# Kernel tuning notes

Hardware: AMD Instinct MI355X
Metric: run time of the kernel (lower is better)

The kernel has to match this reference:

```python
import jax, jax.numpy as jnp
import numpy as np

B, IN, OUT, M = 4096, 512, 512, 16


def setup_inputs() -> dict:
    key = jax.random.key(0)
    k1, k2, k3 = jax.random.split(key, 3)
    # inputs kept strictly positive and inside the physical range [0, 60]
    x = jax.random.uniform(k1, (B, IN), jnp.float32, 0.1, 10.0)
    # photonic basis coefficients: positive, with small polynomial terms
    b_coef = jax.random.uniform(k2, (M, 8), jnp.float32, 0.1, 0.9)
    b_coef = b_coef.at[:, 4:].multiply(0.01)
    coeffs = 0.01 * jax.random.normal(k3, (OUT, IN, M), jnp.float32)
    return {"x": x, "coeffs": coeffs, "b_coef": b_coef}


def _photonic_basis(x, b):
    # x: (B, IN) -> broadcast against M basis functions -> (B, IN, M)
    xe = x[:, :, None]                                   # (B, IN, 1)
    b1, b2, b3, b4, b5, b6, b7, b8 = [b[:, i][None, None, :] for i in range(8)]
    inner = jnp.expm1(b3 * xe)
    powered = jnp.power(inner, b4)
    y = (b1 * jnp.log(1.0 + b2 * jnp.log1p(powered))
         + b5 * xe + b6 * xe**2 + b7 * xe**3 + b8 * xe**4)
    return y


def reference(x, coeffs, b_coef):
    # basis: (B, IN, M); double reduce over (IN, M) == GEMM of size B x (IN*M) x OUT
    basis = _photonic_basis(x, b_coef)
    y = jnp.einsum('bim,oim->bo', basis, coeffs)         # (B, OUT)
    return y
```

## Files before the change

kernel.cpp:

```cpp
#include <hip/hip_runtime.h>
#include <hip/hip_bf16.h>
#include <stdint.h>

#define B_DIM   4096
#define IN_DIM  512
#define OUT_DIM 512
#define M_DIM   16
#define K_DIM   (IN_DIM * M_DIM)
#define MN      (B_DIM * OUT_DIM)

typedef unsigned short ushort_t;
typedef __attribute__((ext_vector_type(8))) __bf16 bf16x8;
typedef __attribute__((ext_vector_type(4))) float  f32x4;

__device__ __forceinline__ ushort_t f2bf(float f) {
  union { float f; uint32_t u; } v; v.f = f;
  uint32_t u = v.u + 0x7fffu + ((v.u >> 16) & 1u);
  return (ushort_t)(u >> 16);
}

__global__ __launch_bounds__(256) void convert_coeffs_kernel(
    const float* __restrict__ src, ushort_t* __restrict__ dst, int n4) {
  int i = blockIdx.x * 256 + threadIdx.x;
  if (i >= n4) return;
  float4 v = ((const float4*)src)[i];
  ushort4 o;
  o.x = f2bf(v.x); o.y = f2bf(v.y); o.z = f2bf(v.z); o.w = f2bf(v.w);
  ((ushort4*)dst)[i] = o;
}

__global__ __launch_bounds__(256) void basis_kernel(
    const float* __restrict__ x, const float* __restrict__ bc,
    ushort_t* __restrict__ basis) {
  int idx = blockIdx.x * 256 + threadIdx.x;
  float xv = x[idx];
  float x2 = xv * xv, x3 = x2 * xv, x4 = x2 * x2;
  const float LOG2E = 1.44269504088896340736f;
  const float LN2   = 0.69314718055994530942f;
  uint32_t w[8];
  #pragma unroll
  for (int m = 0; m < 16; ++m) {
    float b1 = bc[m*8+0], b2 = bc[m*8+1], b3 = bc[m*8+2], b4 = bc[m*8+3];
    float b5 = bc[m*8+4], b6 = bc[m*8+5], b7 = bc[m*8+6], b8 = bc[m*8+7];
    float e     = __builtin_amdgcn_exp2f(b3 * xv * LOG2E);
    float inner = e - 1.0f;
    float p     = __builtin_amdgcn_exp2f(b4 * __builtin_amdgcn_logf(inner));
    float u     = LN2 * __builtin_amdgcn_logf(1.0f + p);
    float vv    = LN2 * __builtin_amdgcn_logf(1.0f + b2 * u);
    float y = b1 * vv + b5 * xv + b6 * x2 + b7 * x3 + b8 * x4;
    uint32_t h = (uint32_t)f2bf(y);
    if (m & 1) w[m >> 1] |= (h << 16); else w[m >> 1] = h;
  }
  uint4* dst = (uint4*)(basis + (size_t)idx * 16);
  dst[0] = make_uint4(w[0], w[1], w[2], w[3]);
  dst[1] = make_uint4(w[4], w[5], w[6], w[7]);
}

#define BM 128
#define BN 128
#define BK 32
#define SPLITK 4
#define KC (K_DIM / SPLITK)

#define GLD16(g, l) \
  __builtin_amdgcn_global_load_lds((const __attribute__((address_space(1))) void*)(g), \
                                   (__attribute__((address_space(3))) void*)(l), 16, 0, 0)

template <int ATOMIC>
__global__ __launch_bounds__(256, 2) void gemm_kernel(
    const ushort_t* __restrict__ A,
    const ushort_t* __restrict__ Bt,
    float* __restrict__ P) {
  __shared__ __align__(16) ushort_t As[BM * BK];
  __shared__ __align__(16) ushort_t Bs[BN * BK];
  const int tid  = threadIdx.x;
  const int wave = tid >> 6;
  const int lane = tid & 63;
  const int bm = blockIdx.x, bn = blockIdx.y, ks = blockIdx.z;

  const int srow = wave * 16 + (lane >> 2);
  const int scol = (lane & 3) * 8;
  const ushort_t* Ag  = A  + (size_t)(bm * BM + srow) * K_DIM + (size_t)ks * KC + scol;
  const ushort_t* Bg  = Bt + (size_t)(bn * BN + srow) * K_DIM + (size_t)ks * KC + scol;
  const ushort_t* Ag2 = Ag + (size_t)64 * K_DIM;
  const ushort_t* Bg2 = Bg + (size_t)64 * K_DIM;
  ushort_t* AsW  = As + wave * 16 * BK;
  ushort_t* AsW2 = AsW + 64 * BK;
  ushort_t* BsW  = Bs + wave * 16 * BK;
  ushort_t* BsW2 = BsW + 64 * BK;

  const int wr = wave >> 1, wc = wave & 1;
  const int fm = lane & 15;
  const int fk = (lane >> 4) * 8;

  f32x4 acc[4][4] = {};

  for (int kt = 0; kt < KC; kt += BK) {
    GLD16(Ag, AsW); GLD16(Ag2, AsW2);
    GLD16(Bg, BsW); GLD16(Bg2, BsW2);
    Ag += BK; Ag2 += BK; Bg += BK; Bg2 += BK;
    __syncthreads();
    bf16x8 af[4], bfv[4];
    #pragma unroll
    for (int t = 0; t < 4; ++t) {
      af[t]  = *(const bf16x8*)(As + (wr * 64 + t * 16 + fm) * BK + fk);
      bfv[t] = *(const bf16x8*)(Bs + (wc * 64 + t * 16 + fm) * BK + fk);
    }
    #pragma unroll
    for (int mt = 0; mt < 4; ++mt)
      #pragma unroll
      for (int nt = 0; nt < 4; ++nt)
        acc[mt][nt] = __builtin_amdgcn_mfma_f32_16x16x32_bf16(af[mt], bfv[nt], acc[mt][nt], 0, 0, 0);
    __syncthreads();
  }

  const int colb = bn * BN + wc * 64 + fm;
  const int rowb = bm * BM + wr * 64 + (lane >> 4) * 4;
  float* out = P + (ATOMIC ? (size_t)0 : (size_t)ks * MN);
  #pragma unroll
  for (int mt = 0; mt < 4; ++mt) {
    #pragma unroll
    for (int nt = 0; nt < 4; ++nt) {
      #pragma unroll
      for (int j = 0; j < 4; ++j) {
        int row = rowb + mt * 16 + j;
        int col = colb + nt * 16;
        float vv = acc[mt][nt][j];
        if (ATOMIC) atomicAdd(out + (size_t)row * OUT_DIM + col, vv);
        else        out[(size_t)row * OUT_DIM + col] = vv;
      }
    }
  }
}

__global__ __launch_bounds__(256) void reduce_kernel(
    const float* __restrict__ P, float* __restrict__ out) {
  int i = blockIdx.x * 256 + threadIdx.x;
  const float4* p = (const float4*)P;
  float4 a = p[i], b = p[i + MN/4], c = p[i + 2*(MN/4)], d = p[i + 3*(MN/4)];
  float4 r = make_float4(a.x + b.x + c.x + d.x, a.y + b.y + c.y + d.y,
                         a.z + b.z + c.z + d.z, a.w + b.w + c.w + d.w);
  ((float4*)out)[i] = r;
}

extern "C" void kernel_launch(void* const* d_in, const int* in_sizes, int n_in,
                              void* d_out, int out_size, void* d_ws, size_t ws_size,
                              hipStream_t stream) {
  const float* x      = (const float*)d_in[0];
  const float* coeffs = (const float*)d_in[1];
  const float* b_coef = (const float*)d_in[2];
  float* out = (float*)d_out;
  char*  ws  = (char*)d_ws;

  const size_t BASIS_BYTES = (size_t)B_DIM * K_DIM * 2;
  const size_t COEF_BYTES  = (size_t)OUT_DIM * K_DIM * 2;
  ushort_t* basis = (ushort_t*)ws;
  ushort_t* coefb = (ushort_t*)(ws + BASIS_BYTES);
  float* partials = (float*)(ws + BASIS_BYTES + COEF_BYTES);
  const size_t FULL = BASIS_BYTES + COEF_BYTES + (size_t)SPLITK * MN * 4;
  const bool use_atomic = (ws_size < FULL);

  convert_coeffs_kernel<<<(OUT_DIM * K_DIM / 4 + 255) / 256, 256, 0, stream>>>(
      coeffs, coefb, OUT_DIM * K_DIM / 4);
  basis_kernel<<<(B_DIM * IN_DIM) / 256, 256, 0, stream>>>(x, b_coef, basis);

  dim3 grid(B_DIM / BM, OUT_DIM / BN, SPLITK);
  if (use_atomic) {
    hipMemsetAsync(d_out, 0, (size_t)MN * 4, stream);
    gemm_kernel<1><<<grid, 256, 0, stream>>>(basis, coefb, out);
  } else {
    gemm_kernel<0><<<grid, 256, 0, stream>>>(basis, coefb, partials);
    reduce_kernel<<<MN / 4 / 256, 256, 0, stream>>>(partials, out);
  }
}
```

Before: 148.3 us.

## Process two inputs per basis thread, raise split-K, remap LDS tile layout

The basis kernel now computes two x values per thread, interleaving their transcendental chains to expose more instruction-level parallelism, and uses half as many threads. The GEMM's LDS layout changes so each wave loads contiguous 16-row by 32-k groups that map directly onto MFMA fragment reads (lane*8), aiming to reduce LDS bank conflicts. Split-K doubles from 4 to 8 to give the GEMM more blocks, and the reduce kernel is generalized to loop over SPLITK. The higher split-K doubles partial-sum traffic and reduce work, or doubles atomic contention on the fallback path.

```diff
diff --git a/kernel.cpp b/kernel.cpp
--- a/kernel.cpp
+++ b/kernel.cpp
@@ -29,37 +29,49 @@
   ((ushort4*)dst)[i] = o;
 }
 
-__global__ __launch_bounds__(256) void basis_kernel(
+__global__ __launch_bounds__(256, 1) void basis_kernel(
     const float* __restrict__ x, const float* __restrict__ bc,
     ushort_t* __restrict__ basis) {
-  int idx = blockIdx.x * 256 + threadIdx.x;
-  float xv = x[idx];
-  float x2 = xv * xv, x3 = x2 * xv, x4 = x2 * x2;
+  int idx2 = blockIdx.x * 256 + threadIdx.x;
+  float2 xp = ((const float2*)x)[idx2];
+  float x0 = xp.x, x1 = xp.y;
+  float p0_2 = x0 * x0, p0_3 = p0_2 * x0, p0_4 = p0_2 * p0_2;
+  float p1_2 = x1 * x1, p1_3 = p1_2 * x1, p1_4 = p1_2 * p1_2;
   const float LOG2E = 1.44269504088896340736f;
   const float LN2   = 0.69314718055994530942f;
-  uint32_t w[8];
+  uint32_t w0[8], w1[8];
   #pragma unroll
   for (int m = 0; m < 16; ++m) {
     float b1 = bc[m*8+0], b2 = bc[m*8+1], b3 = bc[m*8+2], b4 = bc[m*8+3];
     float b5 = bc[m*8+4], b6 = bc[m*8+5], b7 = bc[m*8+6], b8 = bc[m*8+7];
-    float e     = __builtin_amdgcn_exp2f(b3 * xv * LOG2E);
-    float inner = e - 1.0f;
-    float p     = __builtin_amdgcn_exp2f(b4 * __builtin_amdgcn_logf(inner));
-    float u     = LN2 * __builtin_amdgcn_logf(1.0f + p);
-    float vv    = LN2 * __builtin_amdgcn_logf(1.0f + b2 * u);
-    float y = b1 * vv + b5 * xv + b6 * x2 + b7 * x3 + b8 * x4;
-    uint32_t h = (uint32_t)f2bf(y);
-    if (m & 1) w[m >> 1] |= (h << 16); else w[m >> 1] = h;
+    float e0 = __builtin_amdgcn_exp2f(b3 * x0 * LOG2E);
+    float e1 = __builtin_amdgcn_exp2f(b3 * x1 * LOG2E);
+    float l0 = __builtin_amdgcn_logf(e0 - 1.0f);
+    float l1 = __builtin_amdgcn_logf(e1 - 1.0f);
+    float q0 = __builtin_amdgcn_exp2f(b4 * l0);
+    float q1 = __builtin_amdgcn_exp2f(b4 * l1);
+    float u0 = LN2 * __builtin_amdgcn_logf(1.0f + q0);
+    float u1 = LN2 * __builtin_amdgcn_logf(1.0f + q1);
+    float v0 = LN2 * __builtin_amdgcn_logf(1.0f + b2 * u0);
+    float v1 = LN2 * __builtin_amdgcn_logf(1.0f + b2 * u1);
+    float y0 = b1 * v0 + b5 * x0 + b6 * p0_2 + b7 * p0_3 + b8 * p0_4;
+    float y1 = b1 * v1 + b5 * x1 + b6 * p1_2 + b7 * p1_3 + b8 * p1_4;
+    uint32_t h0 = (uint32_t)f2bf(y0);
+    uint32_t h1 = (uint32_t)f2bf(y1);
+    if (m & 1) { w0[m >> 1] |= (h0 << 16); w1[m >> 1] |= (h1 << 16); }
+    else       { w0[m >> 1] = h0;          w1[m >> 1] = h1; }
   }
-  uint4* dst = (uint4*)(basis + (size_t)idx * 16);
-  dst[0] = make_uint4(w[0], w[1], w[2], w[3]);
-  dst[1] = make_uint4(w[4], w[5], w[6], w[7]);
+  uint4* dst = (uint4*)(basis + (size_t)idx2 * 32);
+  dst[0] = make_uint4(w0[0], w0[1], w0[2], w0[3]);
+  dst[1] = make_uint4(w0[4], w0[5], w0[6], w0[7]);
+  dst[2] = make_uint4(w1[0], w1[1], w1[2], w1[3]);
+  dst[3] = make_uint4(w1[4], w1[5], w1[6], w1[7]);
 }
 
 #define BM 128
 #define BN 128
 #define BK 32
-#define SPLITK 4
+#define SPLITK 8
 #define KC (K_DIM / SPLITK)
 
 #define GLD16(g, l) \
@@ -78,33 +90,33 @@
   const int lane = tid & 63;
   const int bm = blockIdx.x, bn = blockIdx.y, ks = blockIdx.z;
 
-  const int srow = wave * 16 + (lane >> 2);
-  const int scol = (lane & 3) * 8;
-  const ushort_t* Ag  = A  + (size_t)(bm * BM + srow) * K_DIM + (size_t)ks * KC + scol;
-  const ushort_t* Bg  = Bt + (size_t)(bn * BN + srow) * K_DIM + (size_t)ks * KC + scol;
-  const ushort_t* Ag2 = Ag + (size_t)64 * K_DIM;
-  const ushort_t* Bg2 = Bg + (size_t)64 * K_DIM;
-  ushort_t* AsW  = As + wave * 16 * BK;
-  ushort_t* AsW2 = AsW + 64 * BK;
-  ushort_t* BsW  = Bs + wave * 16 * BK;
-  ushort_t* BsW2 = BsW + 64 * BK;
+  const int grow = lane & 15;
+  const int koct = lane >> 4;
+  const int g0 = 2 * wave, g1 = 2 * wave + 1;
+  const ushort_t* Ag0 = A  + (size_t)(bm * BM + g0 * 16 + grow) * K_DIM + (size_t)ks * KC + koct * 8;
+  const ushort_t* Ag1 = A  + (size_t)(bm * BM + g1 * 16 + grow) * K_DIM + (size_t)ks * KC + koct * 8;
+  const ushort_t* Bg0 = Bt + (size_t)(bn * BN + g0 * 16 + grow) * K_DIM + (size_t)ks * KC + koct * 8;
+  const ushort_t* Bg1 = Bt + (size_t)(bn * BN + g1 * 16 + grow) * K_DIM + (size_t)ks * KC + koct * 8;
+  ushort_t* AsW0 = As + g0 * 512;
+  ushort_t* AsW1 = As + g1 * 512;
+  ushort_t* BsW0 = Bs + g0 * 512;
+  ushort_t* BsW1 = Bs + g1 * 512;
 
   const int wr = wave >> 1, wc = wave & 1;
   const int fm = lane & 15;
-  const int fk = (lane >> 4) * 8;
 
   f32x4 acc[4][4] = {};
 
   for (int kt = 0; kt < KC; kt += BK) {
-    GLD16(Ag, AsW); GLD16(Ag2, AsW2);
-    GLD16(Bg, BsW); GLD16(Bg2, BsW2);
-    Ag += BK; Ag2 += BK; Bg += BK; Bg2 += BK;
+    GLD16(Ag0, AsW0); GLD16(Ag1, AsW1);
+    GLD16(Bg0, BsW0); GLD16(Bg1, BsW1);
+    Ag0 += BK; Ag1 += BK; Bg0 += BK; Bg1 += BK;
     __syncthreads();
     bf16x8 af[4], bfv[4];
     #pragma unroll
     for (int t = 0; t < 4; ++t) {
-      af[t]  = *(const bf16x8*)(As + (wr * 64 + t * 16 + fm) * BK + fk);
-      bfv[t] = *(const bf16x8*)(Bs + (wc * 64 + t * 16 + fm) * BK + fk);
+      af[t]  = *(const bf16x8*)(As + (wr * 4 + t) * 512 + lane * 8);
+      bfv[t] = *(const bf16x8*)(Bs + (wc * 4 + t) * 512 + lane * 8);
     }
     #pragma unroll
     for (int mt = 0; mt < 4; ++mt)
@@ -137,9 +149,12 @@
     const float* __restrict__ P, float* __restrict__ out) {
   int i = blockIdx.x * 256 + threadIdx.x;
   const float4* p = (const float4*)P;
-  float4 a = p[i], b = p[i + MN/4], c = p[i + 2*(MN/4)], d = p[i + 3*(MN/4)];
-  float4 r = make_float4(a.x + b.x + c.x + d.x, a.y + b.y + c.y + d.y,
-                         a.z + b.z + c.z + d.z, a.w + b.w + c.w + d.w);
+  float4 r = p[i];
+  #pragma unroll
+  for (int s = 1; s < SPLITK; ++s) {
+    float4 t = p[i + (size_t)s * (MN / 4)];
+    r.x += t.x; r.y += t.y; r.z += t.z; r.w += t.w;
+  }
   ((float4*)out)[i] = r;
 }
 
@@ -162,7 +177,7 @@
 
   convert_coeffs_kernel<<<(OUT_DIM * K_DIM / 4 + 255) / 256, 256, 0, stream>>>(
       coeffs, coefb, OUT_DIM * K_DIM / 4);
-  basis_kernel<<<(B_DIM * IN_DIM) / 256, 256, 0, stream>>>(x, b_coef, basis);
+  basis_kernel<<<(B_DIM * IN_DIM / 2) / 256, 256, 0, stream>>>(x, b_coef, basis);
 
   dim3 grid(B_DIM / BM, OUT_DIM / BN, SPLITK);
   if (use_atomic) {
```

Measured after the change: 177.8 us. 1.2x slower.
